# Optimization experiments

Measured on AMD Instinct MI355X. Metric: run time of the kernel, lower is better.

## Reference

```python
import jax, jax.numpy as jnp
import numpy as np

B, Q_LEN, HIST = 1, 2048, 2048
H, KVH, D, HID = 12, 2, 128, 1536
GROUPS = H // KVH  # 6
THETA = 1000000.0


def setup_inputs() -> dict:
    key = jax.random.key(0)
    ks = jax.random.split(key, 8)
    x = jax.random.normal(ks[0], (B, Q_LEN, HID), jnp.float32)
    Wq = jax.random.normal(ks[1], (HID, HID), jnp.float32) * 0.02
    bq = jnp.zeros((HID,), jnp.float32)
    Wk = jax.random.normal(ks[2], (HID, KVH * D), jnp.float32) * 0.02
    bk = jnp.zeros((KVH * D,), jnp.float32)
    Wv = jax.random.normal(ks[3], (HID, KVH * D), jnp.float32) * 0.02
    bv = jnp.zeros((KVH * D,), jnp.float32)
    Wo = jax.random.normal(ks[4], (HID, HID), jnp.float32) * 0.02
    k_hist = jax.random.normal(ks[5], (B, HIST, KVH, D), jnp.float32)
    v_hist = jax.random.normal(ks[6], (B, HIST, KVH, D), jnp.float32)
    # RoPE angles for current-chunk positions [HIST, HIST+Q_LEN)
    inv_freq = 1.0 / (THETA ** (jnp.arange(0, D, 2, dtype=jnp.float32) / D))  # [D/2]
    t = jnp.arange(HIST, HIST + Q_LEN, dtype=jnp.float32)
    ang = t[:, None] * inv_freq[None, :]  # [Q_LEN, D/2]
    return dict(x=x, Wq=Wq, bq=bq, Wk=Wk, bk=bk, Wv=Wv, bv=bv, Wo=Wo,
                k_hist=k_hist, v_hist=v_hist,
                freqs_cos=jnp.cos(ang), freqs_sin=jnp.sin(ang))


def apply_rope(x, cos, sin):
    # x: [B, S, H, D]; cos/sin: [S, D/2]. Split-half rotation (matches torch.polar impl).
    half = D // 2
    x1, x2 = x[..., :half], x[..., half:]
    c = cos[None, :, None, :]
    s = sin[None, :, None, :]
    return jnp.concatenate([x1 * c - x2 * s, x1 * s + x2 * c], axis=-1)


def reference(x, Wq, bq, Wk, bk, Wv, bv, Wo, k_hist, v_hist, freqs_cos, freqs_sin):
    q = (x @ Wq + bq).reshape(B, Q_LEN, H, D)
    k = (x @ Wk + bk).reshape(B, Q_LEN, KVH, D)
    v = (x @ Wv + bv).reshape(B, Q_LEN, KVH, D)
    q = apply_rope(q, freqs_cos, freqs_sin)
    k = apply_rope(k, freqs_cos, freqs_sin)
    # KV-cache concat along sequence dim
    k = jnp.concatenate([k_hist, k], axis=1)  # [B, K_LEN, KVH, D]
    v = jnp.concatenate([v_hist, v], axis=1)
    k_len = HIST + Q_LEN
    # GQA: repeat kv heads (repeat_interleave equivalent along head axis)
    k = jnp.repeat(k, GROUPS, axis=2)  # [B, K_LEN, H, D]
    v = jnp.repeat(v, GROUPS, axis=2)
    scores = jnp.einsum('bqhd,bkhd->bhqk', q, k) / jnp.sqrt(jnp.float32(D))
    # causal mask: triu(-inf, diagonal=k_len - q_len + 1)
    qi = jnp.arange(Q_LEN)[:, None]
    ki = jnp.arange(k_len)[None, :]
    mask = jnp.where(ki > qi + (k_len - Q_LEN), jnp.float32(-jnp.inf), 0.0)
    scores = scores + mask[None, None]
    probs = jax.nn.softmax(scores, axis=-1)
    out = jnp.einsum('bhqk,bkhd->bqhd', probs, v).reshape(B, Q_LEN, HID)
    return out @ Wo
```

## Files before the change

kernel.cpp:

```cpp
#include <hip/hip_runtime.h>
#include <math.h>

#define QL 2048
#define HISTN 2048
#define KLEN 4096
#define NH 12
#define NKVH 2
#define HD 128
#define HID 1536
#define NQKV 2048
#define VTROWS 144
#define QSCALE 0.08838834764831845f

typedef unsigned short u16;
typedef short bf16x8 __attribute__((ext_vector_type(8)));
typedef float f32x4 __attribute__((ext_vector_type(4)));

__device__ __forceinline__ u16 f2bf(float f) {
  union { float f; unsigned u; } v; v.f = f;
  unsigned r = v.u + 0x7FFFu + ((v.u >> 16) & 1u);
  return (u16)(r >> 16);
}
__device__ __forceinline__ float bf2f(u16 h) {
  union { unsigned u; float f; } v; v.u = ((unsigned)h) << 16; return v.f;
}

__device__ __forceinline__ void split_T_tile(const float* __restrict__ W,
    u16* __restrict__ BtH, u16* __restrict__ BtL, int K, int N, int k0, int n0,
    int t, float (*T)[65]) {
  const int r = t >> 4, c = (t & 15) * 4;
#pragma unroll
  for (int p = 0; p < 4; ++p) {
    float4 v = *(const float4*)&W[(size_t)(k0 + p * 16 + r) * N + n0 + c];
    T[p * 16 + r][c + 0] = v.x; T[p * 16 + r][c + 1] = v.y;
    T[p * 16 + r][c + 2] = v.z; T[p * 16 + r][c + 3] = v.w;
  }
  __syncthreads();
  const int rr = t >> 2, cc0 = (t & 3) * 16;
#pragma unroll
  for (int i4 = 0; i4 < 4; ++i4) {
    float f0 = T[cc0 + i4 * 4 + 0][rr];
    float f1 = T[cc0 + i4 * 4 + 1][rr];
    float f2 = T[cc0 + i4 * 4 + 2][rr];
    float f3 = T[cc0 + i4 * 4 + 3][rr];
    ushort4 h, l;
    h.x = f2bf(f0); l.x = f2bf(f0 - bf2f(h.x));
    h.y = f2bf(f1); l.y = f2bf(f1 - bf2f(h.y));
    h.z = f2bf(f2); l.z = f2bf(f2 - bf2f(h.z));
    h.w = f2bf(f3); l.w = f2bf(f3 - bf2f(h.w));
    size_t off = (size_t)(n0 + rr) * K + k0 + cc0 + i4 * 4;
    *(ushort4*)&BtH[off] = h;
    *(ushort4*)&BtL[off] = l;
  }
}

__global__ __launch_bounds__(256) void prep(
    const float* __restrict__ x,  const float* __restrict__ Wq,
    const float* __restrict__ Wk, const float* __restrict__ Wv,
    const float* __restrict__ Wo, const float* __restrict__ bq,
    const float* __restrict__ bk, const float* __restrict__ bv,
    u16* __restrict__ xh, u16* __restrict__ xl,
    u16* __restrict__ WqkvH, u16* __restrict__ WqkvL,
    u16* __restrict__ WoH, u16* __restrict__ WoL, float* __restrict__ bcat) {
  __shared__ float T[64][65];
  const int bx = blockIdx.x, t = threadIdx.x;
  if (bx < 3072) {
    int i = bx * 256 + t;
    float4 v = ((const float4*)x)[i];
    ushort4 h, l;
    h.x = f2bf(v.x); l.x = f2bf(v.x - bf2f(h.x));
    h.y = f2bf(v.y); l.y = f2bf(v.y - bf2f(h.y));
    h.z = f2bf(v.z); l.z = f2bf(v.z - bf2f(h.z));
    h.w = f2bf(v.w); l.w = f2bf(v.w - bf2f(h.w));
    ((ushort4*)xh)[i] = h;
    ((ushort4*)xl)[i] = l;
  } else if (bx < 3648) {
    int b = bx - 3072;
    split_T_tile(Wq, WqkvH, WqkvL, HID, HID, (b / 24) * 64, (b % 24) * 64, t, T);
  } else if (bx < 3744) {
    int b = bx - 3648;
    split_T_tile(Wk, WqkvH + (size_t)HID * HID, WqkvL + (size_t)HID * HID,
                 HID, 256, (b / 4) * 64, (b % 4) * 64, t, T);
  } else if (bx < 3840) {
    int b = bx - 3744;
    split_T_tile(Wv, WqkvH + (size_t)(HID + 256) * HID, WqkvL + (size_t)(HID + 256) * HID,
                 HID, 256, (b / 4) * 64, (b % 4) * 64, t, T);
  } else if (bx < 4416) {
    int b = bx - 3840;
    split_T_tile(Wo, WoH, WoL, HID, HID, (b / 24) * 64, (b % 24) * 64, t, T);
  } else {
    int i = (bx - 4416) * 256 + t;
    bcat[i] = (i < HID) ? bq[i] : (i < HID + 256 ? bk[i - HID] : bv[i - HID - 256]);
  }
}

__global__ __launch_bounds__(256, 2) void gemm3(
    const u16* __restrict__ Ah, const u16* __restrict__ Al,
    const u16* __restrict__ Bh, const u16* __restrict__ Bl,
    const float* __restrict__ bias, float* __restrict__ C,
    int K, int ldc) {
  __shared__ __align__(16) u16 sAh[128 * 64];
  __shared__ __align__(16) u16 sAl[128 * 64];
  __shared__ __align__(16) u16 sBh[64 * 64];
  __shared__ __align__(16) u16 sBl[64 * 64];
  const int m0 = blockIdx.y * 128, n0 = blockIdx.x * 64;
  const int t = threadIdx.x, lane = t & 63, w = t >> 6;
  const int quad = lane >> 4, l15 = lane & 15;
  const int wm = w >> 1, wn = w & 1;
  const int l8 = lane >> 3, j8 = lane & 7;

  f32x4 acc[4][2];
#pragma unroll
  for (int mt = 0; mt < 4; ++mt)
#pragma unroll
    for (int nt = 0; nt < 2; ++nt) acc[mt][nt] = (f32x4){0.f, 0.f, 0.f, 0.f};

  for (int k0 = 0; k0 < K; k0 += 64) {
    if (k0) __syncthreads();
#pragma unroll
    for (int i = 0; i < 4; ++i) {
      int r = (i * 4 + w) * 8 + l8;
      size_t goff = (size_t)(m0 + r) * K + k0 + ((j8 ^ (r & 7)) << 3);
      __builtin_amdgcn_global_load_lds(
          (const __attribute__((address_space(1))) void*)(Ah + goff),
          (__attribute__((address_space(3))) void*)&sAh[(i * 4 + w) * 512], 16, 0, 0);
      __builtin_amdgcn_global_load_lds(
          (const __attribute__((address_space(1))) void*)(Al + goff),
          (__attribute__((address_space(3))) void*)&sAl[(i * 4 + w) * 512], 16, 0, 0);
    }
#pragma unroll
    for (int i = 0; i < 2; ++i) {
      int r = (i * 4 + w) * 8 + l8;
      size_t goff = (size_t)(n0 + r) * K + k0 + ((j8 ^ (r & 7)) << 3);
      __builtin_amdgcn_global_load_lds(
          (const __attribute__((address_space(1))) void*)(Bh + goff),
          (__attribute__((address_space(3))) void*)&sBh[(i * 4 + w) * 512], 16, 0, 0);
      __builtin_amdgcn_global_load_lds(
          (const __attribute__((address_space(1))) void*)(Bl + goff),
          (__attribute__((address_space(3))) void*)&sBl[(i * 4 + w) * 512], 16, 0, 0);
    }
    __syncthreads();
#pragma unroll
    for (int kk = 0; kk < 2; ++kk) {
      bf16x8 aH[4], aL[4], bH[2], bL[2];
#pragma unroll
      for (int mt = 0; mt < 4; ++mt) {
        int r = wm * 64 + mt * 16 + l15;
        int addr = r * 64 + ((((kk << 2) + quad) ^ (r & 7)) << 3);
        aH[mt] = *(const bf16x8*)&sAh[addr];
        aL[mt] = *(const bf16x8*)&sAl[addr];
      }
#pragma unroll
      for (int nt = 0; nt < 2; ++nt) {
        int r = wn * 32 + nt * 16 + l15;
        int addr = r * 64 + ((((kk << 2) + quad) ^ (r & 7)) << 3);
        bH[nt] = *(const bf16x8*)&sBh[addr];
        bL[nt] = *(const bf16x8*)&sBl[addr];
      }
#pragma unroll
      for (int mt = 0; mt < 4; ++mt)
#pragma unroll
        for (int nt = 0; nt < 2; ++nt) {
          acc[mt][nt] = __builtin_amdgcn_mfma_f32_16x16x32_bf16(aH[mt], bH[nt], acc[mt][nt], 0, 0, 0);
          acc[mt][nt] = __builtin_amdgcn_mfma_f32_16x16x32_bf16(aH[mt], bL[nt], acc[mt][nt], 0, 0, 0);
          acc[mt][nt] = __builtin_amdgcn_mfma_f32_16x16x32_bf16(aL[mt], bH[nt], acc[mt][nt], 0, 0, 0);
        }
    }
  }
#pragma unroll
  for (int nt = 0; nt < 2; ++nt) {
    int col = n0 + wn * 32 + nt * 16 + l15;
    float bv = bias ? bias[col] : 0.f;
#pragma unroll
    for (int mt = 0; mt < 4; ++mt)
#pragma unroll
      for (int reg = 0; reg < 4; ++reg) {
        int row = m0 + wm * 64 + mt * 16 + quad * 4 + reg;
        C[(size_t)row * ldc + col] = acc[mt][nt][reg] + bv;
      }
  }
}

__global__ __launch_bounds__(256) void post(
    const float* __restrict__ qkv, const float* __restrict__ k_hist,
    const float* __restrict__ v_hist, const float* __restrict__ cs,
    const float* __restrict__ sn, u16* __restrict__ Qb, u16* __restrict__ Kb,
    u16* __restrict__ Vt) {
  __shared__ u16 T[64][68];
  const int bx = blockIdx.x, t = threadIdx.x;
  if (bx < 1536) {
    int idx = bx * 256 + t;
    int dp4 = (idx & 15) * 4;
    int q   = (idx >> 4) & 2047;
    int h   = idx >> 15;
    const float* base = qkv + (size_t)q * NQKV + h * HD;
    float4 x1 = *(const float4*)&base[dp4];
    float4 x2 = *(const float4*)&base[dp4 + 64];
    float4 c = *(const float4*)&cs[q * 64 + dp4];
    float4 s = *(const float4*)&sn[q * 64 + dp4];
    u16* ob = Qb + ((size_t)h * QL + q) * HD;
    ushort4 o1, o2;
    o1.x = f2bf((x1.x * c.x - x2.x * s.x) * QSCALE);
    o1.y = f2bf((x1.y * c.y - x2.y * s.y) * QSCALE);
    o1.z = f2bf((x1.z * c.z - x2.z * s.z) * QSCALE);
    o1.w = f2bf((x1.w * c.w - x2.w * s.w) * QSCALE);
    o2.x = f2bf((x1.x * s.x + x2.x * c.x) * QSCALE);
    o2.y = f2bf((x1.y * s.y + x2.y * c.y) * QSCALE);
    o2.z = f2bf((x1.z * s.z + x2.z * c.z) * QSCALE);
    o2.w = f2bf((x1.w * s.w + x2.w * c.w) * QSCALE);
    *(ushort4*)&ob[dp4]      = o1;
    *(ushort4*)&ob[dp4 + 64] = o2;
  } else if (bx < 2048) {
    int idx = (bx - 1536) * 256 + t;
    int dp4 = (idx & 15) * 4;
    int tt  = (idx >> 4) & 4095;
    int kvh = idx >> 16;
    u16* ob = Kb + ((size_t)kvh * KLEN + tt) * HD;
    if (tt < HISTN) {
      const float* hb = k_hist + ((size_t)tt * NKVH + kvh) * HD;
      float4 a = *(const float4*)&hb[dp4];
      float4 b = *(const float4*)&hb[dp4 + 64];
      ushort4 o1, o2;
      o1.x = f2bf(a.x); o1.y = f2bf(a.y); o1.z = f2bf(a.z); o1.w = f2bf(a.w);
      o2.x = f2bf(b.x); o2.y = f2bf(b.y); o2.z = f2bf(b.z); o2.w = f2bf(b.w);
      *(ushort4*)&ob[dp4]      = o1;
      *(ushort4*)&ob[dp4 + 64] = o2;
    } else {
      int q = tt - HISTN;
      const float* base = qkv + (size_t)q * NQKV + HID + kvh * HD;
      float4 x1 = *(const float4*)&base[dp4];
      float4 x2 = *(const float4*)&base[dp4 + 64];
      float4 c = *(const float4*)&cs[q * 64 + dp4];
      float4 s = *(const float4*)&sn[q * 64 + dp4];
      ushort4 o1, o2;
      o1.x = f2bf(x1.x * c.x - x2.x * s.x);
      o1.y = f2bf(x1.y * c.y - x2.y * s.y);
      o1.z = f2bf(x1.z * c.z - x2.z * s.z);
      o1.w = f2bf(x1.w * c.w - x2.w * s.w);
      o2.x = f2bf(x1.x * s.x + x2.x * c.x);
      o2.y = f2bf(x1.y * s.y + x2.y * c.y);
      o2.z = f2bf(x1.z * s.z + x2.z * c.z);
      o2.w = f2bf(x1.w * s.w + x2.w * c.w);
      *(ushort4*)&ob[dp4]      = o1;
      *(ushort4*)&ob[dp4 + 64] = o2;
    }
  } else {
    int b = bx - 2048;
    int xt = b % 65, rest = b / 65;
    int dh = rest & 1, kvh = rest >> 1;
    if (xt == 64) {
      int r0 = 128 + dh * 8;
      u16* base = Vt + ((size_t)kvh * VTROWS) * KLEN;
      for (int i = t; i < 8192; i += 256) {
        int row = r0 + (i >> 10), c4 = (i & 1023) * 4;
        u16 v = (row == 128) ? (u16)0x3F80 : (u16)0;
        ushort4 o4 = {v, v, v, v};
        *(ushort4*)&base[(size_t)row * KLEN + c4] = o4;
      }
      return;
    }
    const int t0 = xt * 64, d0 = dh * 64;
    const int r = t >> 4, c = (t & 15) * 4;
#pragma unroll
    for (int p = 0; p < 4; ++p) {
      int tt = t0 + p * 16 + r;
      float4 v;
      if (tt < HISTN) v = *(const float4*)&v_hist[((size_t)tt * NKVH + kvh) * HD + d0 + c];
      else            v = *(const float4*)&qkv[(size_t)(tt - HISTN) * NQKV + HID + 256 + kvh * HD + d0 + c];
      T[p * 16 + r][c + 0] = f2bf(v.x); T[p * 16 + r][c + 1] = f2bf(v.y);
      T[p * 16 + r][c + 2] = f2bf(v.z); T[p * 16 + r][c + 3] = f2bf(v.w);
    }
    __syncthreads();
    const int dr = t >> 2, cc0 = (t & 3) * 16;
#pragma unroll
    for (int i4 = 0; i4 < 4; ++i4) {
      ushort4 o4;
      o4.x = T[cc0 + i4 * 4 + 0][dr];
      o4.y = T[cc0 + i4 * 4 + 1][dr];
      o4.z = T[cc0 + i4 * 4 + 2][dr];
      o4.w = T[cc0 + i4 * 4 + 3][dr];
      *(ushort4*)&Vt[((size_t)kvh * VTROWS + d0 + dr) * KLEN + t0 + cc0 + i4 * 4] = o4;
    }
  }
}

__global__ __launch_bounds__(384, 2) void attn6(
    const u16* __restrict__ Q, const u16* __restrict__ K,
    const u16* __restrict__ Vt, float* __restrict__ oacc) {
  __shared__ __align__(16) u16 sK[2][64 * 128];
  __shared__ __align__(16) u16 sV[2][128 * 64];
  __shared__ __align__(16) u16 sP[6][2304];
  const int bid = blockIdx.x;
  const int kvh   = (bid >> 2) & 1;
  const int qs    = (bid & 3) | ((bid >> 3) << 2);
  const int qt    = qs >> 2, slice = qs & 3;
  const int q0 = qt * 32;
  const int t = threadIdx.x, lane = t & 63, w = t / 64;
  const int h = kvh * 6 + w;
  const int quad = lane >> 4, l15 = lane & 15, q8 = quad * 8;

  const u16* Qg = Q + ((size_t)h * QL + q0) * HD;
  bf16x8 Qf[2][4];
#pragma unroll
  for (int mt = 0; mt < 2; ++mt)
#pragma unroll
    for (int dc = 0; dc < 4; ++dc)
      Qf[mt][dc] = *(const bf16x8*)&Qg[(mt * 16 + l15) * HD + dc * 32 + q8];

  const int nsteps = (q0 + 32 + HISTN + 63) >> 6;
  const int bas = nsteps >> 2, rem = nsteps & 3;
  const int cnt = bas + (slice < rem ? 1 : 0);
  const int s0  = slice * bas + (slice < rem ? slice : rem);

  f32x4 o[2][8], ol[2];
#pragma unroll
  for (int mt = 0; mt < 2; ++mt) {
    ol[mt] = (f32x4){0.f, 0.f, 0.f, 0.f};
#pragma unroll
    for (int dt = 0; dt < 8; ++dt) o[mt][dt] = (f32x4){0.f, 0.f, 0.f, 0.f};
  }

  bf16x8 onesf;
  {
    short v = (l15 == 0) ? (short)0x3F80 : (short)0;
#pragma unroll
    for (int j = 0; j < 8; ++j) onesf[j] = v;
  }

  const u16* Kh = K + (size_t)kvh * KLEN * HD;
  const u16* Vh = Vt + (size_t)kvh * VTROWS * KLEN;
  u16* sPw = sP[w];
  const int x7 = l15 & 7;

  auto STAGE = [&](int b, int k0) {
    for (int i = w; i < 32; i += 6) {
      if (i < 16) {
        int r = 4 * i + (lane >> 4);
        int c = lane & 15;
        const u16* src = Kh + (size_t)(k0 + r) * HD + ((c ^ (r & 7)) << 3);
        __builtin_amdgcn_global_load_lds(
            (const __attribute__((address_space(1))) void*)src,
            (__attribute__((address_space(3))) void*)&sK[b][i * 512], 16, 0, 0);
      } else {
        int j = i - 16;
        int r = 8 * j + (lane >> 3);
        int c = lane & 7;
        const u16* src = Vh + (size_t)r * KLEN + k0 + ((c ^ (r & 7)) << 3);
        __builtin_amdgcn_global_load_lds(
            (const __attribute__((address_space(1))) void*)src,
            (__attribute__((address_space(3))) void*)&sV[b][j * 512], 16, 0, 0);
      }
    }
  };

  int cur = 0;
  STAGE(0, s0 << 6);
  __syncthreads();

  for (int s = s0; s < s0 + cnt; ++s) {
    const int k0 = s << 6;
    if (s + 1 < s0 + cnt) STAGE(cur ^ 1, (s + 1) << 6);
    f32x4 sc[2][4];
#pragma unroll
    for (int mt = 0; mt < 2; ++mt)
#pragma unroll
      for (int kt = 0; kt < 4; ++kt) sc[mt][kt] = (f32x4){0.f, 0.f, 0.f, 0.f};
#pragma unroll
    for (int dc = 0; dc < 4; ++dc) {
      bf16x8 bK[4];
#pragma unroll
      for (int kt = 0; kt < 4; ++kt)
        bK[kt] = *(const bf16x8*)&sK[cur][(kt * 16 + l15) * 128 + (((dc * 4 + quad) ^ x7) << 3)];
#pragma unroll
      for (int mt = 0; mt < 2; ++mt)
#pragma unroll
        for (int kt = 0; kt < 4; ++kt)
          sc[mt][kt] = __builtin_amdgcn_mfma_f32_16x16x32_bf16(Qf[mt][dc], bK[kt], sc[mt][kt], 0, 0, 0);
    }
    if (k0 + 63 - HISTN > q0) {
#pragma unroll
      for (int mt = 0; mt < 2; ++mt)
#pragma unroll
        for (int kt = 0; kt < 4; ++kt) {
          int kg = k0 + kt * 16 + l15;
#pragma unroll
          for (int reg = 0; reg < 4; ++reg)
            if (kg > q0 + mt * 16 + quad * 4 + reg + HISTN) sc[mt][kt][reg] = -INFINITY;
        }
    }
#pragma unroll
    for (int mt = 0; mt < 2; ++mt)
#pragma unroll
      for (int reg = 0; reg < 4; ++reg)
#pragma unroll
        for (int kt = 0; kt < 4; ++kt) {
          float p = __expf(sc[mt][kt][reg]);
          sPw[(mt * 16 + quad * 4 + reg) * 72 + kt * 16 + l15] = f2bf(p);
        }
#pragma unroll
    for (int kc = 0; kc < 2; ++kc) {
      bf16x8 aP[2];
#pragma unroll
      for (int mt = 0; mt < 2; ++mt)
        aP[mt] = *(const bf16x8*)&sPw[(mt * 16 + l15) * 72 + kc * 32 + q8];
#pragma unroll
      for (int dt = 0; dt < 8; ++dt) {
        bf16x8 bV = *(const bf16x8*)&sV[cur][(dt * 16 + l15) * 64 + (((kc * 4 + quad) ^ x7) << 3)];
#pragma unroll
        for (int mt = 0; mt < 2; ++mt)
          o[mt][dt] = __builtin_amdgcn_mfma_f32_16x16x32_bf16(aP[mt], bV, o[mt][dt], 0, 0, 0);
      }
#pragma unroll
      for (int mt = 0; mt < 2; ++mt)
        ol[mt] = __builtin_amdgcn_mfma_f32_16x16x32_bf16(aP[mt], onesf, ol[mt], 0, 0, 0);
    }
    __syncthreads();
    cur ^= 1;
  }

  float* ob = oacc + ((size_t)h * QL + q0) * 132;
#pragma unroll
  for (int mt = 0; mt < 2; ++mt)
#pragma unroll
    for (int reg = 0; reg < 4; ++reg) {
      int r = mt * 16 + quad * 4 + reg;
#pragma unroll
      for (int dt = 0; dt < 8; ++dt)
        atomicAdd(&ob[(size_t)r * 132 + dt * 16 + l15], o[mt][dt][reg]);
      if (l15 == 0) atomicAdd(&ob[(size_t)r * 132 + 128], ol[mt][reg]);
    }
}

__global__ __launch_bounds__(256) void attn_norm(const float* __restrict__ oacc,
    u16* __restrict__ OH, u16* __restrict__ OL) {
  int fi = blockIdx.x * 256 + threadIdx.x;
  int d4 = fi & 31;
  int q  = (fi >> 5) & 2047;
  int h  = fi >> 16;
  const float* row = oacc + ((size_t)h * QL + q) * 132;
  float inv = 1.f / row[128];
  float4 v = *(const float4*)&row[d4 * 4];
  size_t ob = (size_t)q * HID + h * HD + d4 * 4;
  float vals[4] = {v.x, v.y, v.z, v.w};
#pragma unroll
  for (int j = 0; j < 4; ++j) {
    float val = vals[j] * inv;
    u16 hv = f2bf(val);
    OH[ob + j] = hv;
    OL[ob + j] = f2bf(val - bf2f(hv));
  }
}

extern "C" void kernel_launch(void* const* d_in, const int* in_sizes, int n_in,
                              void* d_out, int out_size, void* d_ws, size_t ws_size,
                              hipStream_t stream) {
  (void)in_sizes; (void)n_in; (void)out_size; (void)ws_size;
  const float* x      = (const float*)d_in[0];
  const float* Wq     = (const float*)d_in[1];
  const float* bq     = (const float*)d_in[2];
  const float* Wk     = (const float*)d_in[3];
  const float* bk     = (const float*)d_in[4];
  const float* Wv     = (const float*)d_in[5];
  const float* bv     = (const float*)d_in[6];
  const float* Wo     = (const float*)d_in[7];
  const float* k_hist = (const float*)d_in[8];
  const float* v_hist = (const float*)d_in[9];
  const float* fcos   = (const float*)d_in[10];
  const float* fsin   = (const float*)d_in[11];
  float* out = (float*)d_out;

  char* p = (char*)d_ws;
  float* qkv   = (float*)p;  p += (size_t)QL * NQKV * 4;
  u16*   Qb    = (u16*)p;    p += (size_t)NH * QL * HD * 2;
  u16*   Kb    = (u16*)p;    p += (size_t)NKVH * KLEN * HD * 2;
  u16*   Vtb   = (u16*)p;    p += (size_t)NKVH * VTROWS * KLEN * 2;
  u16*   xh    = (u16*)p;    p += (size_t)QL * HID * 2;
  u16*   xl    = (u16*)p;    p += (size_t)QL * HID * 2;
  u16*   WqkvH = (u16*)p;    p += (size_t)NQKV * HID * 2;
  u16*   WqkvL = (u16*)p;    p += (size_t)NQKV * HID * 2;
  u16*   WoH   = (u16*)p;    p += (size_t)HID * HID * 2;
  u16*   WoL   = (u16*)p;    p += (size_t)HID * HID * 2;
  float* bcat  = (float*)p;  p += (size_t)NQKV * 4;
  u16* attnH = xh;  u16* attnL = xl;
  float* oacc = qkv;

  prep<<<4424, 256, 0, stream>>>(x, Wq, Wk, Wv, Wo, bq, bk, bv,
                                 xh, xl, WqkvH, WqkvL, WoH, WoL, bcat);
  gemm3<<<dim3(NQKV / 64, QL / 128), 256, 0, stream>>>(xh, xl, WqkvH, WqkvL, bcat, qkv, HID, NQKV);
  post<<<2308, 256, 0, stream>>>(qkv, k_hist, v_hist, fcos, fsin, Qb, Kb, Vtb);
  hipMemsetAsync(oacc, 0, (size_t)NH * QL * 132 * 4, stream);
  attn6<<<512, 384, 0, stream>>>(Qb, Kb, Vtb, oacc);
  attn_norm<<<3072, 256, 0, stream>>>(oacc, attnH, attnL);
  gemm3<<<dim3(HID / 64, QL / 128), 256, 0, stream>>>(attnH, attnL, WoH, WoL, nullptr, out, HID, HID);
}
```

Measured before the change: 313.1 us.

## Read K and V fragments directly from global memory instead of LDS staging

Removes the double-buffered LDS staging of K and V tiles and the per-iteration block barrier. Each wave now loads its MFMA B-operand fragments straight from global memory, which shrinks shared memory use so occupancy can rise to three blocks per CU. The cost is that six waves redundantly fetch the same K/V data through L1/L2, and global-load latency is no longer hidden by the async prefetch.

```diff
diff --git a/kernel.cpp b/kernel.cpp
--- a/kernel.cpp
+++ b/kernel.cpp
@@ -284,11 +284,9 @@
   }
 }
 
-__global__ __launch_bounds__(384, 2) void attn6(
+__global__ __launch_bounds__(384, 3) void attn6(
     const u16* __restrict__ Q, const u16* __restrict__ K,
     const u16* __restrict__ Vt, float* __restrict__ oacc) {
-  __shared__ __align__(16) u16 sK[2][64 * 128];
-  __shared__ __align__(16) u16 sV[2][128 * 64];
   __shared__ __align__(16) u16 sP[6][2304];
   const int bid = blockIdx.x;
   const int kvh   = (bid >> 2) & 1;
@@ -330,36 +328,9 @@
   const u16* Kh = K + (size_t)kvh * KLEN * HD;
   const u16* Vh = Vt + (size_t)kvh * VTROWS * KLEN;
   u16* sPw = sP[w];
-  const int x7 = l15 & 7;
-
-  auto STAGE = [&](int b, int k0) {
-    for (int i = w; i < 32; i += 6) {
-      if (i < 16) {
-        int r = 4 * i + (lane >> 4);
-        int c = lane & 15;
-        const u16* src = Kh + (size_t)(k0 + r) * HD + ((c ^ (r & 7)) << 3);
-        __builtin_amdgcn_global_load_lds(
-            (const __attribute__((address_space(1))) void*)src,
-            (__attribute__((address_space(3))) void*)&sK[b][i * 512], 16, 0, 0);
-      } else {
-        int j = i - 16;
-        int r = 8 * j + (lane >> 3);
-        int c = lane & 7;
-        const u16* src = Vh + (size_t)r * KLEN + k0 + ((c ^ (r & 7)) << 3);
-        __builtin_amdgcn_global_load_lds(
-            (const __attribute__((address_space(1))) void*)src,
-            (__attribute__((address_space(3))) void*)&sV[b][j * 512], 16, 0, 0);
-      }
-    }
-  };
-
-  int cur = 0;
-  STAGE(0, s0 << 6);
-  __syncthreads();
 
   for (int s = s0; s < s0 + cnt; ++s) {
     const int k0 = s << 6;
-    if (s + 1 < s0 + cnt) STAGE(cur ^ 1, (s + 1) << 6);
     f32x4 sc[2][4];
 #pragma unroll
     for (int mt = 0; mt < 2; ++mt)
@@ -370,7 +341,7 @@
       bf16x8 bK[4];
 #pragma unroll
       for (int kt = 0; kt < 4; ++kt)
-        bK[kt] = *(const bf16x8*)&sK[cur][(kt * 16 + l15) * 128 + (((dc * 4 + quad) ^ x7) << 3)];
+        bK[kt] = *(const bf16x8*)&Kh[(size_t)(k0 + kt * 16 + l15) * HD + dc * 32 + q8];
 #pragma unroll
       for (int mt = 0; mt < 2; ++mt)
 #pragma unroll
@@ -405,7 +376,7 @@
         aP[mt] = *(const bf16x8*)&sPw[(mt * 16 + l15) * 72 + kc * 32 + q8];
 #pragma unroll
       for (int dt = 0; dt < 8; ++dt) {
-        bf16x8 bV = *(const bf16x8*)&sV[cur][(dt * 16 + l15) * 64 + (((kc * 4 + quad) ^ x7) << 3)];
+        bf16x8 bV = *(const bf16x8*)&Vh[(size_t)(dt * 16 + l15) * KLEN + k0 + kc * 32 + q8];
 #pragma unroll
         for (int mt = 0; mt < 2; ++mt)
           o[mt][dt] = __builtin_amdgcn_mfma_f32_16x16x32_bf16(aP[mt], bV, o[mt][dt], 0, 0, 0);
@@ -414,8 +385,6 @@
       for (int mt = 0; mt < 2; ++mt)
         ol[mt] = __builtin_amdgcn_mfma_f32_16x16x32_bf16(aP[mt], onesf, ol[mt], 0, 0, 0);
     }
-    __syncthreads();
-    cur ^= 1;
   }
 
   float* ob = oacc + ((size_t)h * QL + q0) * 132;
```

After: 418.6 us. 1.34x slower.

## Keep attention probabilities in registers via transposed MFMA and lane shuffles

Applied to the files above, without the earlier changes.

Swaps the MFMA operand order so score tiles come out transposed, with each lane holding one query row. The exponentiated probabilities are packed to bf16 with v_cvt_pk_bf16 and rearranged with cross-lane shuffles into the PV operand layout, replacing the per-wave shared-memory round trip for P. The row sum is now a register accumulation plus shuffle reduction instead of an extra MFMA against a ones vector. Dropping the sP shared buffer lets launch bounds request 3 blocks per CU, at the cost of more register pressure and shuffle traffic.

```diff
diff --git a/kernel.cpp b/kernel.cpp
--- a/kernel.cpp
+++ b/kernel.cpp
@@ -23,6 +23,11 @@
 }
 __device__ __forceinline__ float bf2f(u16 h) {
   union { unsigned u; float f; } v; v.u = ((unsigned)h) << 16; return v.f;
+}
+__device__ __forceinline__ unsigned cvt_pk_bf16(float lo, float hi) {
+  unsigned d;
+  asm("v_cvt_pk_bf16_f32 %0, %1, %2" : "=v"(d) : "v"(lo), "v"(hi));
+  return d;
 }
 
 __device__ __forceinline__ void split_T_tile(const float* __restrict__ W,
@@ -284,12 +289,11 @@
   }
 }
 
-__global__ __launch_bounds__(384, 2) void attn6(
+__global__ __launch_bounds__(384, 3) void attn6(
     const u16* __restrict__ Q, const u16* __restrict__ K,
     const u16* __restrict__ Vt, float* __restrict__ oacc) {
   __shared__ __align__(16) u16 sK[2][64 * 128];
   __shared__ __align__(16) u16 sV[2][128 * 64];
-  __shared__ __align__(16) u16 sP[6][2304];
   const int bid = blockIdx.x;
   const int kvh   = (bid >> 2) & 1;
   const int qs    = (bid & 3) | ((bid >> 3) << 2);
@@ -312,24 +316,15 @@
   const int cnt = bas + (slice < rem ? 1 : 0);
   const int s0  = slice * bas + (slice < rem ? slice : rem);
 
-  f32x4 o[2][8], ol[2];
-#pragma unroll
-  for (int mt = 0; mt < 2; ++mt) {
-    ol[mt] = (f32x4){0.f, 0.f, 0.f, 0.f};
+  f32x4 o[2][8];
+  float lp[2] = {0.f, 0.f};
+#pragma unroll
+  for (int mt = 0; mt < 2; ++mt)
 #pragma unroll
     for (int dt = 0; dt < 8; ++dt) o[mt][dt] = (f32x4){0.f, 0.f, 0.f, 0.f};
-  }
-
-  bf16x8 onesf;
-  {
-    short v = (l15 == 0) ? (short)0x3F80 : (short)0;
-#pragma unroll
-    for (int j = 0; j < 8; ++j) onesf[j] = v;
-  }
 
   const u16* Kh = K + (size_t)kvh * KLEN * HD;
   const u16* Vh = Vt + (size_t)kvh * VTROWS * KLEN;
-  u16* sPw = sP[w];
   const int x7 = l15 & 7;
 
   auto STAGE = [&](int b, int k0) {
@@ -375,44 +370,61 @@
       for (int mt = 0; mt < 2; ++mt)
 #pragma unroll
         for (int kt = 0; kt < 4; ++kt)
-          sc[mt][kt] = __builtin_amdgcn_mfma_f32_16x16x32_bf16(Qf[mt][dc], bK[kt], sc[mt][kt], 0, 0, 0);
+          sc[mt][kt] = __builtin_amdgcn_mfma_f32_16x16x32_bf16(bK[kt], Qf[mt][dc], sc[mt][kt], 0, 0, 0);
     }
     if (k0 + 63 - HISTN > q0) {
 #pragma unroll
       for (int mt = 0; mt < 2; ++mt)
 #pragma unroll
         for (int kt = 0; kt < 4; ++kt) {
-          int kg = k0 + kt * 16 + l15;
-#pragma unroll
-          for (int reg = 0; reg < 4; ++reg)
-            if (kg > q0 + mt * 16 + quad * 4 + reg + HISTN) sc[mt][kt][reg] = -INFINITY;
+#pragma unroll
+          for (int reg = 0; reg < 4; ++reg) {
+            int kg = k0 + kt * 16 + quad * 4 + reg;
+            if (kg > q0 + mt * 16 + l15 + HISTN) sc[mt][kt][reg] = -INFINITY;
+          }
         }
     }
 #pragma unroll
     for (int mt = 0; mt < 2; ++mt)
 #pragma unroll
-      for (int reg = 0; reg < 4; ++reg)
-#pragma unroll
-        for (int kt = 0; kt < 4; ++kt) {
+      for (int kt = 0; kt < 4; ++kt)
+#pragma unroll
+        for (int reg = 0; reg < 4; ++reg) {
           float p = __expf(sc[mt][kt][reg]);
-          sPw[(mt * 16 + quad * 4 + reg) * 72 + kt * 16 + l15] = f2bf(p);
+          sc[mt][kt][reg] = p;
+          lp[mt] += p;
         }
 #pragma unroll
     for (int kc = 0; kc < 2; ++kc) {
-      bf16x8 aP[2];
-#pragma unroll
-      for (int mt = 0; mt < 2; ++mt)
-        aP[mt] = *(const bf16x8*)&sPw[(mt * 16 + l15) * 72 + kc * 32 + q8];
+      bf16x8 pP[2];
+#pragma unroll
+      for (int mt = 0; mt < 2; ++mt) {
+        const f32x4 pa = sc[mt][kc * 2];
+        const f32x4 pb = sc[mt][kc * 2 + 1];
+        unsigned A0 = cvt_pk_bf16(pa[0], pa[1]);
+        unsigned A1 = cvt_pk_bf16(pa[2], pa[3]);
+        unsigned B0 = cvt_pk_bf16(pb[0], pb[1]);
+        unsigned B1 = cvt_pk_bf16(pb[2], pb[3]);
+        bool hiQ = quad >= 2;
+        unsigned s16a = hiQ ? B0 : A0, s16b = hiQ ? B1 : A1;
+        unsigned s3a  = hiQ ? A0 : B0, s3b  = hiQ ? A1 : B1;
+        unsigned r16a = __shfl_xor(s16a, 16), r16b = __shfl_xor(s16b, 16);
+        unsigned r32a = __shfl_xor(s3a, 32),  r32b = __shfl_xor(s3b, 32);
+        unsigned r48a = __shfl_xor(s3a, 48),  r48b = __shfl_xor(s3b, 48);
+        union { unsigned u[4]; bf16x8 v; } P;
+        P.u[0] = quad == 0 ? A0 : quad == 1 ? r48a : quad == 2 ? r32a : r16a;
+        P.u[1] = quad == 0 ? A1 : quad == 1 ? r48b : quad == 2 ? r32b : r16b;
+        P.u[2] = quad == 0 ? r16a : quad == 1 ? r32a : quad == 2 ? r48a : B0;
+        P.u[3] = quad == 0 ? r16b : quad == 1 ? r32b : quad == 2 ? r48b : B1;
+        pP[mt] = P.v;
+      }
 #pragma unroll
       for (int dt = 0; dt < 8; ++dt) {
         bf16x8 bV = *(const bf16x8*)&sV[cur][(dt * 16 + l15) * 64 + (((kc * 4 + quad) ^ x7) << 3)];
 #pragma unroll
         for (int mt = 0; mt < 2; ++mt)
-          o[mt][dt] = __builtin_amdgcn_mfma_f32_16x16x32_bf16(aP[mt], bV, o[mt][dt], 0, 0, 0);
-      }
-#pragma unroll
-      for (int mt = 0; mt < 2; ++mt)
-        ol[mt] = __builtin_amdgcn_mfma_f32_16x16x32_bf16(aP[mt], onesf, ol[mt], 0, 0, 0);
+          o[mt][dt] = __builtin_amdgcn_mfma_f32_16x16x32_bf16(bV, pP[mt], o[mt][dt], 0, 0, 0);
+      }
     }
     __syncthreads();
     cur ^= 1;
@@ -420,15 +432,17 @@
 
   float* ob = oacc + ((size_t)h * QL + q0) * 132;
 #pragma unroll
-  for (int mt = 0; mt < 2; ++mt)
-#pragma unroll
-    for (int reg = 0; reg < 4; ++reg) {
-      int r = mt * 16 + quad * 4 + reg;
-#pragma unroll
-      for (int dt = 0; dt < 8; ++dt)
-        atomicAdd(&ob[(size_t)r * 132 + dt * 16 + l15], o[mt][dt][reg]);
-      if (l15 == 0) atomicAdd(&ob[(size_t)r * 132 + 128], ol[mt][reg]);
-    }
+  for (int mt = 0; mt < 2; ++mt) {
+    lp[mt] += __shfl_xor(lp[mt], 16);
+    lp[mt] += __shfl_xor(lp[mt], 32);
+    int r = mt * 16 + l15;
+#pragma unroll
+    for (int dt = 0; dt < 8; ++dt)
+#pragma unroll
+      for (int reg = 0; reg < 4; ++reg)
+        atomicAdd(&ob[(size_t)r * 132 + dt * 16 + quad * 4 + reg], o[mt][dt][reg]);
+    if (quad == 0) atomicAdd(&ob[(size_t)r * 132 + 128], lp[mt]);
+  }
 }
 
 __global__ __launch_bounds__(256) void attn_norm(const float* __restrict__ oacc,
```

New measurement: 520.8 us. 66.4% more time.
